# Kernel tuning notes

Hardware: AMD Instinct MI355X
Metric: run time of the kernel (lower is better)

## Reference

```python
import jax, jax.numpy as jnp
import numpy as np

B, C, H, W = 8, 96, 512, 96  # W == w_size (required by the view semantics)
EPS = 1e-5


def setup_inputs() -> dict:
    key = jax.random.key(0)
    ks = jax.random.split(key, 3)
    x = jax.random.normal(ks[0], (B, C, H, W), dtype=jnp.float32)
    bn_gamma = jnp.ones((C,), jnp.float32)
    bn_beta = jnp.zeros((C,), jnp.float32)
    bn_mean = jnp.zeros((C,), jnp.float32)   # BatchNorm running mean (eval mode)
    bn_var = jnp.ones((C,), jnp.float32)     # BatchNorm running var  (eval mode)
    qkv_w = jax.random.normal(ks[1], (3 * C, C), jnp.float32) * (1.0 / np.sqrt(C))
    qkv_b = jnp.zeros((3 * C,), jnp.float32)
    return {"x": x, "bn_gamma": bn_gamma, "bn_beta": bn_beta,
            "bn_mean": bn_mean, "bn_var": bn_var,
            "qkv_w": qkv_w, "qkv_b": qkv_b}


def reference(x, bn_gamma, bn_beta, bn_mean, bn_var, qkv_w, qkv_b):
    # BatchNorm2d (eval-mode affine normalize), fused scale/shift per channel
    inv = (bn_gamma / jnp.sqrt(bn_var + EPS))[:, None, None]
    xn = (x - bn_mean[:, None, None]) * inv + bn_beta[:, None, None]
    # 1x1 conv QKV projection: [b,c,h,w] -> [b,3c,h,w]
    qkv = jnp.einsum('bchw,oc->bohw', xn, qkv_w) + qkv_b[None, :, None, None]
    q, k, v = jnp.split(qkv, 3, axis=1)  # each [b,c,h,w]
    # per-row attention over the width axis (w == w_size)
    qp = jnp.transpose(q, (0, 2, 3, 1))  # [b,h,w,c]
    kp = jnp.transpose(k, (0, 2, 3, 1))  # [b,h,w,c]
    vp = jnp.transpose(v, (0, 2, 3, 1))  # [b,h,w,c]
    score = jnp.einsum('bhqc,bhkc->bhqk', qp, kp)  # [b,h,w,w]
    attn = jax.nn.softmax(score, axis=-1)
    xt = jnp.einsum('bhqk,bhkc->bhqc', attn, vp)   # [b,h,w,c]
    out = jnp.transpose(xt, (0, 3, 1, 2)) + x       # residual add, [b,c,h,w]
    return out
```

## Files before the change

kernel.cpp:

```cpp
#include <hip/hip_runtime.h>

#define C_ 96
#define H_ 512
#define W_ 96
#define HW_ 49152
#define CHW_ 4718592
#define PIT 104
#define REG 9984

typedef _Float16 f16x8 __attribute__((ext_vector_type(8)));
typedef _Float16 f16x4 __attribute__((ext_vector_type(4)));
typedef _Float16 f16x2 __attribute__((ext_vector_type(2)));
typedef float    f32x4 __attribute__((ext_vector_type(4)));
typedef int      i32x4 __attribute__((ext_vector_type(4)));

#define MFMA16 __builtin_amdgcn_mfma_f32_16x16x32_f16

#define BAR() do { __builtin_amdgcn_sched_barrier(0); \
                   asm volatile("s_waitcnt lgkmcnt(0)" ::: "memory"); \
                   __builtin_amdgcn_s_barrier(); \
                   __builtin_amdgcn_sched_barrier(0); } while (0)

__global__ void prep_kernel(const float* __restrict__ wq,
                            const float* __restrict__ gamma,
                            const float* __restrict__ beta,
                            const float* __restrict__ mean,
                            const float* __restrict__ var,
                            const float* __restrict__ qkvb,
                            _Float16* __restrict__ whf,
                            float* __restrict__ bprime)
{
    int i = blockIdx.x * 256 + threadIdx.x;
    if (i < 3 * C_ * C_) {
        int c = i % C_;
        float iv = gamma[c] * rsqrtf(var[c] + 1e-5f);
        whf[i] = (_Float16)(wq[i] * iv);
    }
    if (i < 3 * C_) {
        float acc = qkvb[i];
        for (int c = 0; c < C_; ++c) {
            float iv = gamma[c] * rsqrtf(var[c] + 1e-5f);
            acc += wq[i * C_ + c] * (beta[c] - mean[c] * iv);
        }
        bprime[i] = acc;
    }
}

__global__ void prep2_kernel(const float* __restrict__ wq,
                             const float* __restrict__ gamma,
                             const float* __restrict__ var,
                             const float* __restrict__ bprime,
                             _Float16* __restrict__ atm,
                             float* __restrict__ g0)
{
    int i = blockIdx.x * 256 + threadIdx.x;
    if (i >= 9216) return;
    int c = i / 96, cp = i % 96;
    float ivc  = gamma[c]  * rsqrtf(var[c]  + 1e-5f);
    float ivcp = gamma[cp] * rsqrtf(var[cp] + 1e-5f);
    float acc = 0.f;
    #pragma unroll 4
    for (int o = 0; o < 96; ++o)
        acc += wq[o * 96 + cp] * wq[(96 + o) * 96 + c];
    atm[c * 96 + cp] = (_Float16)(acc * ivc * ivcp);
    if (cp == 0) {
        float a2 = 0.f;
        #pragma unroll 4
        for (int o = 0; o < 96; ++o)
            a2 += bprime[o] * wq[(96 + o) * 96 + c];
        g0[c] = a2 * ivc;
    }
}

__device__ __forceinline__ void xchg(const f32x4 v[6], float scale,
                                     int q4, int n16, f16x8 fr[3])
{
    int pq[6][2];
    #pragma unroll
    for (int nt = 0; nt < 6; ++nt) {
        #pragma unroll
        for (int jj = 0; jj < 2; ++jj) {
            f16x2 h;
            h[0] = (_Float16)(v[nt][2 * jj] * scale);
            h[1] = (_Float16)(v[nt][2 * jj + 1] * scale);
            pq[nt][jj] = __builtin_bit_cast(int, h);
        }
    }
    const int srcA = ((q4 & 1) << 5) | n16;
    const int srcB = srcA + 16;
    #pragma unroll
    for (int kk = 0; kk < 3; ++kk) {
        const int a0 = __shfl(pq[2 * kk][0], srcA), a1 = __shfl(pq[2 * kk][1], srcA);
        const int a2 = __shfl(pq[2 * kk][0], srcB), a3 = __shfl(pq[2 * kk][1], srcB);
        const int b0 = __shfl(pq[2 * kk + 1][0], srcA), b1 = __shfl(pq[2 * kk + 1][1], srcA);
        const int b2 = __shfl(pq[2 * kk + 1][0], srcB), b3 = __shfl(pq[2 * kk + 1][1], srcB);
        i32x4 u;
        u[0] = (q4 < 2) ? a0 : b0;
        u[1] = (q4 < 2) ? a1 : b1;
        u[2] = (q4 < 2) ? a2 : b2;
        u[3] = (q4 < 2) ? a3 : b3;
        fr[kk] = __builtin_bit_cast(f16x8, u);
    }
}

__global__ __launch_bounds__(384, 5) void attn_kernel(
    const float* __restrict__ x,
    const _Float16* __restrict__ whf,
    const _Float16* __restrict__ atm,
    const float* __restrict__ g0,
    const float* __restrict__ bprime,
    float* __restrict__ out)
{
    __shared__ __align__(16) _Float16 smem[2 * REG];
    _Float16* XN  = smem;
    _Float16* XNT = smem + REG;

    const int tid  = threadIdx.x;
    const int ws   = tid >> 6;
    const int lane = tid & 63;
    const int q4   = lane >> 4;
    const int n16  = lane & 15;
    const int w0   = 16 * ws + 4 * q4;
    const int qrow = 16 * ws + n16;

    const int bh = blockIdx.x;
    const size_t base = (size_t)(bh >> 9) * CHW_ + (size_t)(bh & 511) * W_;

    {
        f32x4 xr[6];
        #pragma unroll
        for (int t = 0; t < 6; ++t)
            xr[t] = *(const f32x4*)(x + base + (size_t)(16 * t + n16) * HW_ + w0);
        #pragma unroll
        for (int t = 0; t < 6; ++t) {
            const int c = 16 * t + n16;
            f16x4 pk;
            #pragma unroll
            for (int r = 0; r < 4; ++r) pk[r] = (_Float16)xr[t][r];
            *(f16x4*)(XNT + c * PIT + w0) = pk;
            #pragma unroll
            for (int r = 0; r < 4; ++r)
                XN[(w0 + r) * PIT + c] = (_Float16)xr[t][r];
        }
    }
    BAR();

    f32x4 gac[6];
    #pragma unroll
    for (int nt = 0; nt < 6; ++nt)
        gac[nt] = *(const f32x4*)(g0 + 16 * nt + 4 * q4);
    #pragma unroll
    for (int kk = 0; kk < 3; ++kk) {
        const f16x8 bfr = *(const f16x8*)(XN + qrow * PIT + 32 * kk + 8 * q4);
        #pragma unroll
        for (int nt = 0; nt < 6; ++nt) {
            const f16x8 afr = *(const f16x8*)(atm + (16 * nt + n16) * 96 + 32 * kk + 8 * q4);
            gac[nt] = MFMA16(afr, bfr, gac[nt], 0, 0, 0);
        }
    }
    f16x8 gf[3];
    xchg(gac, 1.0f, q4, n16, gf);

    f32x4 sacc[6];
    #pragma unroll
    for (int nt = 0; nt < 6; ++nt) sacc[nt] = f32x4{0.f, 0.f, 0.f, 0.f};
    #pragma unroll
    for (int kk = 0; kk < 3; ++kk) {
        #pragma unroll
        for (int nt = 0; nt < 6; ++nt) {
            const f16x8 afr = *(const f16x8*)(XN + (16 * nt + n16) * PIT + 32 * kk + 8 * q4);
            sacc[nt] = MFMA16(afr, gf[kk], sacc[nt], 0, 0, 0);
        }
    }

    float mr0 = sacc[0][0], mr1 = sacc[0][1], mr2 = sacc[0][2], mr3 = sacc[0][3];
    #pragma unroll
    for (int nt = 1; nt < 6; ++nt) {
        mr0 = fmaxf(mr0, sacc[nt][0]); mr1 = fmaxf(mr1, sacc[nt][1]);
        mr2 = fmaxf(mr2, sacc[nt][2]); mr3 = fmaxf(mr3, sacc[nt][3]);
    }
    float m = fmaxf(fmaxf(mr0, mr1), fmaxf(mr2, mr3));
    m = fmaxf(m, __shfl_xor(m, 16));
    m = fmaxf(m, __shfl_xor(m, 32));
    float sr0 = 0.f, sr1 = 0.f, sr2 = 0.f, sr3 = 0.f;
    #pragma unroll
    for (int nt = 0; nt < 6; ++nt) {
        sacc[nt][0] = __expf(sacc[nt][0] - m); sr0 += sacc[nt][0];
        sacc[nt][1] = __expf(sacc[nt][1] - m); sr1 += sacc[nt][1];
        sacc[nt][2] = __expf(sacc[nt][2] - m); sr2 += sacc[nt][2];
        sacc[nt][3] = __expf(sacc[nt][3] - m); sr3 += sacc[nt][3];
    }
    float s = (sr0 + sr1) + (sr2 + sr3);
    s += __shfl_xor(s, 16);
    s += __shfl_xor(s, 32);
    const float pinv = 1.0f / s;

    f16x8 pa[3];
    xchg(sacc, pinv, q4, n16, pa);

    float xv[6][4];
    #pragma unroll
    for (int ot = 0; ot < 6; ++ot)
        #pragma unroll
        for (int r = 0; r < 4; ++r)
            xv[ot][r] = x[base + (size_t)(16 * ot + 4 * q4 + r) * HW_ + qrow];

    f32x4 zac[6];
    #pragma unroll
    for (int nt = 0; nt < 6; ++nt) zac[nt] = f32x4{0.f, 0.f, 0.f, 0.f};
    #pragma unroll
    for (int kk = 0; kk < 3; ++kk) {
        #pragma unroll
        for (int nt = 0; nt < 6; ++nt) {
            const f16x8 afr = *(const f16x8*)(XNT + (16 * nt + n16) * PIT + 32 * kk + 8 * q4);
            zac[nt] = MFMA16(afr, pa[kk], zac[nt], 0, 0, 0);
        }
    }
    f16x8 zf[3];
    xchg(zac, 1.0f, q4, n16, zf);

    f32x4 oacc[6];
    #pragma unroll
    for (int ot = 0; ot < 6; ++ot)
        oacc[ot] = *(const f32x4*)(bprime + 192 + 16 * ot + 4 * q4);
    #pragma unroll
    for (int kk = 0; kk < 3; ++kk) {
        #pragma unroll
        for (int ot = 0; ot < 6; ++ot) {
            const f16x8 afr = *(const f16x8*)(whf + (192 + 16 * ot + n16) * 96 + 32 * kk + 8 * q4);
            oacc[ot] = MFMA16(afr, zf[kk], oacc[ot], 0, 0, 0);
        }
    }

    #pragma unroll
    for (int ot = 0; ot < 6; ++ot)
        #pragma unroll
        for (int r = 0; r < 4; ++r)
            out[base + (size_t)(16 * ot + 4 * q4 + r) * HW_ + qrow] =
                oacc[ot][r] + xv[ot][r];
}

extern "C" void kernel_launch(void* const* d_in, const int* in_sizes, int n_in,
                              void* d_out, int out_size, void* d_ws, size_t ws_size,
                              hipStream_t stream)
{
    const float* x     = (const float*)d_in[0];
    const float* gamma = (const float*)d_in[1];
    const float* beta  = (const float*)d_in[2];
    const float* mean  = (const float*)d_in[3];
    const float* var   = (const float*)d_in[4];
    const float* qkvw  = (const float*)d_in[5];
    const float* qkvb  = (const float*)d_in[6];
    float* out = (float*)d_out;

    _Float16* whf    = (_Float16*)d_ws;
    float*    bprime = (float*)((char*)d_ws + 55296);
    _Float16* atm    = (_Float16*)((char*)d_ws + 56448);
    float*    g0v    = (float*)((char*)d_ws + 74880);

    prep_kernel<<<108, 256, 0, stream>>>(qkvw, gamma, beta, mean, var, qkvb, whf, bprime);
    prep2_kernel<<<36, 256, 0, stream>>>(qkvw, gamma, var, bprime, atm, g0v);
    attn_kernel<<<4096, 384, 0, stream>>>(x, whf, atm, g0v, bprime, out);
}
```

Baseline: 366.1 us.

## Switch to 16x16x16 MFMA so accumulator layouts feed next stage without shuffles

Replaces the 16x16x32 f16 MFMA chain with the 16x16x16 variant. Its output accumulator layout matches the B-operand layout of the next MFMA, so the cross-lane shuffle exchange (xchg) between the four GEMM stages becomes a plain f32-to-f16 conversion in registers. It also double-buffers the global weight-fragment loads for the first and last GEMMs. The cost is twice as many MFMA instructions and smaller 8-byte LDS and global fragment loads in exchange for removing the shuffles.

```diff
diff --git a/kernel.cpp b/kernel.cpp
--- a/kernel.cpp
+++ b/kernel.cpp
@@ -10,11 +10,9 @@
 
 typedef _Float16 f16x8 __attribute__((ext_vector_type(8)));
 typedef _Float16 f16x4 __attribute__((ext_vector_type(4)));
-typedef _Float16 f16x2 __attribute__((ext_vector_type(2)));
 typedef float    f32x4 __attribute__((ext_vector_type(4)));
-typedef int      i32x4 __attribute__((ext_vector_type(4)));
-
-#define MFMA16 __builtin_amdgcn_mfma_f32_16x16x32_f16
+
+#define MFMA16K __builtin_amdgcn_mfma_f32_16x16x16f16
 
 #define BAR() do { __builtin_amdgcn_sched_barrier(0); \
                    asm volatile("s_waitcnt lgkmcnt(0)" ::: "memory"); \
@@ -59,47 +57,16 @@
     float ivc  = gamma[c]  * rsqrtf(var[c]  + 1e-5f);
     float ivcp = gamma[cp] * rsqrtf(var[cp] + 1e-5f);
     float acc = 0.f;
-    #pragma unroll 4
+    #pragma unroll 8
     for (int o = 0; o < 96; ++o)
         acc += wq[o * 96 + cp] * wq[(96 + o) * 96 + c];
     atm[c * 96 + cp] = (_Float16)(acc * ivc * ivcp);
     if (cp == 0) {
         float a2 = 0.f;
-        #pragma unroll 4
+        #pragma unroll 8
         for (int o = 0; o < 96; ++o)
             a2 += bprime[o] * wq[(96 + o) * 96 + c];
         g0[c] = a2 * ivc;
-    }
-}
-
-__device__ __forceinline__ void xchg(const f32x4 v[6], float scale,
-                                     int q4, int n16, f16x8 fr[3])
-{
-    int pq[6][2];
-    #pragma unroll
-    for (int nt = 0; nt < 6; ++nt) {
-        #pragma unroll
-        for (int jj = 0; jj < 2; ++jj) {
-            f16x2 h;
-            h[0] = (_Float16)(v[nt][2 * jj] * scale);
-            h[1] = (_Float16)(v[nt][2 * jj + 1] * scale);
-            pq[nt][jj] = __builtin_bit_cast(int, h);
-        }
-    }
-    const int srcA = ((q4 & 1) << 5) | n16;
-    const int srcB = srcA + 16;
-    #pragma unroll
-    for (int kk = 0; kk < 3; ++kk) {
-        const int a0 = __shfl(pq[2 * kk][0], srcA), a1 = __shfl(pq[2 * kk][1], srcA);
-        const int a2 = __shfl(pq[2 * kk][0], srcB), a3 = __shfl(pq[2 * kk][1], srcB);
-        const int b0 = __shfl(pq[2 * kk + 1][0], srcA), b1 = __shfl(pq[2 * kk + 1][1], srcA);
-        const int b2 = __shfl(pq[2 * kk + 1][0], srcB), b3 = __shfl(pq[2 * kk + 1][1], srcB);
-        i32x4 u;
-        u[0] = (q4 < 2) ? a0 : b0;
-        u[1] = (q4 < 2) ? a1 : b1;
-        u[2] = (q4 < 2) ? a2 : b2;
-        u[3] = (q4 < 2) ? a3 : b3;
-        fr[kk] = __builtin_bit_cast(f16x8, u);
     }
 }
 
@@ -147,29 +114,43 @@
 
     f32x4 gac[6];
     #pragma unroll
-    for (int nt = 0; nt < 6; ++nt)
-        gac[nt] = *(const f32x4*)(g0 + 16 * nt + 4 * q4);
-    #pragma unroll
-    for (int kk = 0; kk < 3; ++kk) {
-        const f16x8 bfr = *(const f16x8*)(XN + qrow * PIT + 32 * kk + 8 * q4);
+    for (int ct = 0; ct < 6; ++ct)
+        gac[ct] = *(const f32x4*)(g0 + 16 * ct + 4 * q4);
+    {
+        f16x4 atf[2][6];
+        #pragma unroll
+        for (int ct = 0; ct < 6; ++ct)
+            atf[0][ct] = *(const f16x4*)(atm + (16 * ct + n16) * 96 + 4 * q4);
+        #pragma unroll
+        for (int kk = 0; kk < 6; ++kk) {
+            if (kk < 5) {
+                #pragma unroll
+                for (int ct = 0; ct < 6; ++ct)
+                    atf[(kk + 1) & 1][ct] =
+                        *(const f16x4*)(atm + (16 * ct + n16) * 96 + 16 * (kk + 1) + 4 * q4);
+            }
+            const f16x4 bq = *(const f16x4*)(XN + qrow * PIT + 16 * kk + 4 * q4);
+            #pragma unroll
+            for (int ct = 0; ct < 6; ++ct)
+                gac[ct] = MFMA16K(atf[kk & 1][ct], bq, gac[ct], 0, 0, 0);
+        }
+    }
+    f16x4 gf[6];
+    #pragma unroll
+    for (int ct = 0; ct < 6; ++ct) {
+        #pragma unroll
+        for (int r = 0; r < 4; ++r) gf[ct][r] = (_Float16)gac[ct][r];
+    }
+
+    f32x4 sacc[6];
+    #pragma unroll
+    for (int nt = 0; nt < 6; ++nt) sacc[nt] = f32x4{0.f, 0.f, 0.f, 0.f};
+    #pragma unroll
+    for (int kk = 0; kk < 6; ++kk) {
         #pragma unroll
         for (int nt = 0; nt < 6; ++nt) {
-            const f16x8 afr = *(const f16x8*)(atm + (16 * nt + n16) * 96 + 32 * kk + 8 * q4);
-            gac[nt] = MFMA16(afr, bfr, gac[nt], 0, 0, 0);
-        }
-    }
-    f16x8 gf[3];
-    xchg(gac, 1.0f, q4, n16, gf);
-
-    f32x4 sacc[6];
-    #pragma unroll
-    for (int nt = 0; nt < 6; ++nt) sacc[nt] = f32x4{0.f, 0.f, 0.f, 0.f};
-    #pragma unroll
-    for (int kk = 0; kk < 3; ++kk) {
-        #pragma unroll
-        for (int nt = 0; nt < 6; ++nt) {
-            const f16x8 afr = *(const f16x8*)(XN + (16 * nt + n16) * PIT + 32 * kk + 8 * q4);
-            sacc[nt] = MFMA16(afr, gf[kk], sacc[nt], 0, 0, 0);
+            const f16x4 a = *(const f16x4*)(XN + (16 * nt + n16) * PIT + 16 * kk + 4 * q4);
+            sacc[nt] = MFMA16K(a, gf[kk], sacc[nt], 0, 0, 0);
         }
     }
 
@@ -194,9 +175,30 @@
     s += __shfl_xor(s, 16);
     s += __shfl_xor(s, 32);
     const float pinv = 1.0f / s;
-
-    f16x8 pa[3];
-    xchg(sacc, pinv, q4, n16, pa);
+    f16x4 pb[6];
+    #pragma unroll
+    for (int kk = 0; kk < 6; ++kk) {
+        #pragma unroll
+        for (int r = 0; r < 4; ++r) pb[kk][r] = (_Float16)(sacc[kk][r] * pinv);
+    }
+
+    f32x4 zac[6];
+    #pragma unroll
+    for (int nt = 0; nt < 6; ++nt) zac[nt] = f32x4{0.f, 0.f, 0.f, 0.f};
+    #pragma unroll
+    for (int kk = 0; kk < 6; ++kk) {
+        #pragma unroll
+        for (int nt = 0; nt < 6; ++nt) {
+            const f16x4 a = *(const f16x4*)(XNT + (16 * nt + n16) * PIT + 16 * kk + 4 * q4);
+            zac[nt] = MFMA16K(a, pb[kk], zac[nt], 0, 0, 0);
+        }
+    }
+    f16x4 zf[6];
+    #pragma unroll
+    for (int ct = 0; ct < 6; ++ct) {
+        #pragma unroll
+        for (int r = 0; r < 4; ++r) zf[ct][r] = (_Float16)zac[ct][r];
+    }
 
     float xv[6][4];
     #pragma unroll
@@ -205,30 +207,26 @@
         for (int r = 0; r < 4; ++r)
             xv[ot][r] = x[base + (size_t)(16 * ot + 4 * q4 + r) * HW_ + qrow];
 
-    f32x4 zac[6];
-    #pragma unroll
-    for (int nt = 0; nt < 6; ++nt) zac[nt] = f32x4{0.f, 0.f, 0.f, 0.f};
-    #pragma unroll
-    for (int kk = 0; kk < 3; ++kk) {
-        #pragma unroll
-        for (int nt = 0; nt < 6; ++nt) {
-            const f16x8 afr = *(const f16x8*)(XNT + (16 * nt + n16) * PIT + 32 * kk + 8 * q4);
-            zac[nt] = MFMA16(afr, pa[kk], zac[nt], 0, 0, 0);
-        }
-    }
-    f16x8 zf[3];
-    xchg(zac, 1.0f, q4, n16, zf);
-
     f32x4 oacc[6];
     #pragma unroll
     for (int ot = 0; ot < 6; ++ot)
         oacc[ot] = *(const f32x4*)(bprime + 192 + 16 * ot + 4 * q4);
-    #pragma unroll
-    for (int kk = 0; kk < 3; ++kk) {
-        #pragma unroll
-        for (int ot = 0; ot < 6; ++ot) {
-            const f16x8 afr = *(const f16x8*)(whf + (192 + 16 * ot + n16) * 96 + 32 * kk + 8 * q4);
-            oacc[ot] = MFMA16(afr, zf[kk], oacc[ot], 0, 0, 0);
+    {
+        f16x4 wvf[2][6];
+        #pragma unroll
+        for (int ot = 0; ot < 6; ++ot)
+            wvf[0][ot] = *(const f16x4*)(whf + (192 + 16 * ot + n16) * 96 + 4 * q4);
+        #pragma unroll
+        for (int kk = 0; kk < 6; ++kk) {
+            if (kk < 5) {
+                #pragma unroll
+                for (int ot = 0; ot < 6; ++ot)
+                    wvf[(kk + 1) & 1][ot] =
+                        *(const f16x4*)(whf + (192 + 16 * ot + n16) * 96 + 16 * (kk + 1) + 4 * q4);
+            }
+            #pragma unroll
+            for (int ot = 0; ot < 6; ++ot)
+                oacc[ot] = MFMA16K(wvf[kk & 1][ot], zf[kk], oacc[ot], 0, 0, 0);
         }
     }
 
```

After: 407.5 us. +11.3%, slower.

## Process eight rows per block with double-buffered LDS and register-resident weights

Applied to the files above, without the earlier changes.

Each workgroup now handles eight consecutive h-rows instead of one. The next row's x is prefetched into registers during the current row's compute and staged into a second LDS buffer. The atm fragments are hoisted into registers once per block, and the residual is read from the fp16 LDS copy instead of reloading x from global memory. The aim is to amortise setup and hide global-load latency, at the cost of far fewer blocks (lower occupancy), higher register pressure, and reduced residual precision.

```diff
diff --git a/kernel.cpp b/kernel.cpp
--- a/kernel.cpp
+++ b/kernel.cpp
@@ -7,6 +7,7 @@
 #define CHW_ 4718592
 #define PIT 104
 #define REG 9984
+#define TILES 8
 
 typedef _Float16 f16x8 __attribute__((ext_vector_type(8)));
 typedef _Float16 f16x4 __attribute__((ext_vector_type(4)));
@@ -59,13 +60,13 @@
     float ivc  = gamma[c]  * rsqrtf(var[c]  + 1e-5f);
     float ivcp = gamma[cp] * rsqrtf(var[cp] + 1e-5f);
     float acc = 0.f;
-    #pragma unroll 4
+    #pragma unroll 8
     for (int o = 0; o < 96; ++o)
         acc += wq[o * 96 + cp] * wq[(96 + o) * 96 + c];
     atm[c * 96 + cp] = (_Float16)(acc * ivc * ivcp);
     if (cp == 0) {
         float a2 = 0.f;
-        #pragma unroll 4
+        #pragma unroll 8
         for (int o = 0; o < 96; ++o)
             a2 += bprime[o] * wq[(96 + o) * 96 + c];
         g0[c] = a2 * ivc;
@@ -103,7 +104,7 @@
     }
 }
 
-__global__ __launch_bounds__(384, 5) void attn_kernel(
+__global__ __launch_bounds__(384, 3) void attn_kernel(
     const float* __restrict__ x,
     const _Float16* __restrict__ whf,
     const _Float16* __restrict__ atm,
@@ -111,9 +112,7 @@
     const float* __restrict__ bprime,
     float* __restrict__ out)
 {
-    __shared__ __align__(16) _Float16 smem[2 * REG];
-    _Float16* XN  = smem;
-    _Float16* XNT = smem + REG;
+    __shared__ __align__(16) _Float16 smem[4 * REG];
 
     const int tid  = threadIdx.x;
     const int ws   = tid >> 6;
@@ -123,121 +122,155 @@
     const int w0   = 16 * ws + 4 * q4;
     const int qrow = 16 * ws + n16;
 
-    const int bh = blockIdx.x;
-    const size_t base = (size_t)(bh >> 9) * CHW_ + (size_t)(bh & 511) * W_;
+    const int wg = blockIdx.x;
+    size_t base = (size_t)(wg >> 6) * CHW_ + (size_t)((wg & 63) * TILES) * W_;
+
+    f16x8 atf[3][6];
+    #pragma unroll
+    for (int kk = 0; kk < 3; ++kk)
+        #pragma unroll
+        for (int nt = 0; nt < 6; ++nt)
+            atf[kk][nt] = *(const f16x8*)(atm + (16 * nt + n16) * 96 + 32 * kk + 8 * q4);
 
     {
         f32x4 xr[6];
         #pragma unroll
-        for (int t = 0; t < 6; ++t)
-            xr[t] = *(const f32x4*)(x + base + (size_t)(16 * t + n16) * HW_ + w0);
-        #pragma unroll
-        for (int t = 0; t < 6; ++t) {
-            const int c = 16 * t + n16;
+        for (int t6 = 0; t6 < 6; ++t6)
+            xr[t6] = *(const f32x4*)(x + base + (size_t)(16 * t6 + n16) * HW_ + w0);
+        #pragma unroll
+        for (int t6 = 0; t6 < 6; ++t6) {
+            const int c = 16 * t6 + n16;
             f16x4 pk;
             #pragma unroll
-            for (int r = 0; r < 4; ++r) pk[r] = (_Float16)xr[t][r];
-            *(f16x4*)(XNT + c * PIT + w0) = pk;
+            for (int r = 0; r < 4; ++r) pk[r] = (_Float16)xr[t6][r];
+            *(f16x4*)(smem + REG + c * PIT + w0) = pk;
             #pragma unroll
             for (int r = 0; r < 4; ++r)
-                XN[(w0 + r) * PIT + c] = (_Float16)xr[t][r];
+                smem[(w0 + r) * PIT + c] = (_Float16)xr[t6][r];
         }
     }
     BAR();
 
-    f32x4 gac[6];
-    #pragma unroll
-    for (int nt = 0; nt < 6; ++nt)
-        gac[nt] = *(const f32x4*)(g0 + 16 * nt + 4 * q4);
-    #pragma unroll
-    for (int kk = 0; kk < 3; ++kk) {
-        const f16x8 bfr = *(const f16x8*)(XN + qrow * PIT + 32 * kk + 8 * q4);
+    #pragma unroll 2
+    for (int t = 0; t < TILES; ++t) {
+        _Float16* XNc  = smem + ((t & 1) ? 2 * REG : 0);
+        _Float16* XNTc = XNc + REG;
+        _Float16* XNn  = smem + ((t & 1) ? 0 : 2 * REG);
+        _Float16* XNTn = XNn + REG;
+
+        f32x4 gac[6];
+        #pragma unroll
+        for (int nt = 0; nt < 6; ++nt)
+            gac[nt] = *(const f32x4*)(g0 + 16 * nt + 4 * q4);
+        #pragma unroll
+        for (int kk = 0; kk < 3; ++kk) {
+            const f16x8 bq = *(const f16x8*)(XNc + qrow * PIT + 32 * kk + 8 * q4);
+            #pragma unroll
+            for (int nt = 0; nt < 6; ++nt)
+                gac[nt] = MFMA16(atf[kk][nt], bq, gac[nt], 0, 0, 0);
+        }
+        f16x8 gf[3];
+        xchg(gac, 1.0f, q4, n16, gf);
+
+        f32x4 sacc[6];
+        #pragma unroll
+        for (int nt = 0; nt < 6; ++nt) sacc[nt] = f32x4{0.f, 0.f, 0.f, 0.f};
+        #pragma unroll
+        for (int kk = 0; kk < 3; ++kk) {
+            #pragma unroll
+            for (int nt = 0; nt < 6; ++nt) {
+                const f16x8 a = *(const f16x8*)(XNc + (16 * nt + n16) * PIT + 32 * kk + 8 * q4);
+                sacc[nt] = MFMA16(a, gf[kk], sacc[nt], 0, 0, 0);
+            }
+        }
+
+        float mr0 = sacc[0][0], mr1 = sacc[0][1], mr2 = sacc[0][2], mr3 = sacc[0][3];
+        #pragma unroll
+        for (int nt = 1; nt < 6; ++nt) {
+            mr0 = fmaxf(mr0, sacc[nt][0]); mr1 = fmaxf(mr1, sacc[nt][1]);
+            mr2 = fmaxf(mr2, sacc[nt][2]); mr3 = fmaxf(mr3, sacc[nt][3]);
+        }
+        float m = fmaxf(fmaxf(mr0, mr1), fmaxf(mr2, mr3));
+        m = fmaxf(m, __shfl_xor(m, 16));
+        m = fmaxf(m, __shfl_xor(m, 32));
+        float sr0 = 0.f, sr1 = 0.f, sr2 = 0.f, sr3 = 0.f;
         #pragma unroll
         for (int nt = 0; nt < 6; ++nt) {
-            const f16x8 afr = *(const f16x8*)(atm + (16 * nt + n16) * 96 + 32 * kk + 8 * q4);
-            gac[nt] = MFMA16(afr, bfr, gac[nt], 0, 0, 0);
-        }
-    }
-    f16x8 gf[3];
-    xchg(gac, 1.0f, q4, n16, gf);
-
-    f32x4 sacc[6];
-    #pragma unroll
-    for (int nt = 0; nt < 6; ++nt) sacc[nt] = f32x4{0.f, 0.f, 0.f, 0.f};
-    #pragma unroll
-    for (int kk = 0; kk < 3; ++kk) {
-        #pragma unroll
-        for (int nt = 0; nt < 6; ++nt) {
-            const f16x8 afr = *(const f16x8*)(XN + (16 * nt + n16) * PIT + 32 * kk + 8 * q4);
-            sacc[nt] = MFMA16(afr, gf[kk], sacc[nt], 0, 0, 0);
-        }
-    }
-
-    float mr0 = sacc[0][0], mr1 = sacc[0][1], mr2 = sacc[0][2], mr3 = sacc[0][3];
-    #pragma unroll
-    for (int nt = 1; nt < 6; ++nt) {
-        mr0 = fmaxf(mr0, sacc[nt][0]); mr1 = fmaxf(mr1, sacc[nt][1]);
-        mr2 = fmaxf(mr2, sacc[nt][2]); mr3 = fmaxf(mr3, sacc[nt][3]);
-    }
-    float m = fmaxf(fmaxf(mr0, mr1), fmaxf(mr2, mr3));
-    m = fmaxf(m, __shfl_xor(m, 16));
-    m = fmaxf(m, __shfl_xor(m, 32));
-    float sr0 = 0.f, sr1 = 0.f, sr2 = 0.f, sr3 = 0.f;
-    #pragma unroll
-    for (int nt = 0; nt < 6; ++nt) {
-        sacc[nt][0] = __expf(sacc[nt][0] - m); sr0 += sacc[nt][0];
-        sacc[nt][1] = __expf(sacc[nt][1] - m); sr1 += sacc[nt][1];
-        sacc[nt][2] = __expf(sacc[nt][2] - m); sr2 += sacc[nt][2];
-        sacc[nt][3] = __expf(sacc[nt][3] - m); sr3 += sacc[nt][3];
-    }
-    float s = (sr0 + sr1) + (sr2 + sr3);
-    s += __shfl_xor(s, 16);
-    s += __shfl_xor(s, 32);
-    const float pinv = 1.0f / s;
-
-    f16x8 pa[3];
-    xchg(sacc, pinv, q4, n16, pa);
-
-    float xv[6][4];
-    #pragma unroll
-    for (int ot = 0; ot < 6; ++ot)
-        #pragma unroll
-        for (int r = 0; r < 4; ++r)
-            xv[ot][r] = x[base + (size_t)(16 * ot + 4 * q4 + r) * HW_ + qrow];
-
-    f32x4 zac[6];
-    #pragma unroll
-    for (int nt = 0; nt < 6; ++nt) zac[nt] = f32x4{0.f, 0.f, 0.f, 0.f};
-    #pragma unroll
-    for (int kk = 0; kk < 3; ++kk) {
-        #pragma unroll
-        for (int nt = 0; nt < 6; ++nt) {
-            const f16x8 afr = *(const f16x8*)(XNT + (16 * nt + n16) * PIT + 32 * kk + 8 * q4);
-            zac[nt] = MFMA16(afr, pa[kk], zac[nt], 0, 0, 0);
-        }
-    }
-    f16x8 zf[3];
-    xchg(zac, 1.0f, q4, n16, zf);
-
-    f32x4 oacc[6];
-    #pragma unroll
-    for (int ot = 0; ot < 6; ++ot)
-        oacc[ot] = *(const f32x4*)(bprime + 192 + 16 * ot + 4 * q4);
-    #pragma unroll
-    for (int kk = 0; kk < 3; ++kk) {
+            sacc[nt][0] = __expf(sacc[nt][0] - m); sr0 += sacc[nt][0];
+            sacc[nt][1] = __expf(sacc[nt][1] - m); sr1 += sacc[nt][1];
+            sacc[nt][2] = __expf(sacc[nt][2] - m); sr2 += sacc[nt][2];
+            sacc[nt][3] = __expf(sacc[nt][3] - m); sr3 += sacc[nt][3];
+        }
+        float s = (sr0 + sr1) + (sr2 + sr3);
+        s += __shfl_xor(s, 16);
+        s += __shfl_xor(s, 32);
+        const float pinv = 1.0f / s;
+        f16x8 pa[3];
+        xchg(sacc, pinv, q4, n16, pa);
+
+        f32x4 xrn[6];
+        if (t < TILES - 1) {
+            #pragma unroll
+            for (int t6 = 0; t6 < 6; ++t6)
+                xrn[t6] = *(const f32x4*)(x + base + W_
+                              + (size_t)(16 * t6 + n16) * HW_ + w0);
+        }
+
+        f32x4 zac[6];
+        #pragma unroll
+        for (int nt = 0; nt < 6; ++nt) zac[nt] = f32x4{0.f, 0.f, 0.f, 0.f};
+        #pragma unroll
+        for (int kk = 0; kk < 3; ++kk) {
+            #pragma unroll
+            for (int nt = 0; nt < 6; ++nt) {
+                const f16x8 a = *(const f16x8*)(XNTc + (16 * nt + n16) * PIT + 32 * kk + 8 * q4);
+                zac[nt] = MFMA16(a, pa[kk], zac[nt], 0, 0, 0);
+            }
+        }
+        f16x8 zf[3];
+        xchg(zac, 1.0f, q4, n16, zf);
+
+        f32x4 oacc[6];
+        #pragma unroll
+        for (int ot = 0; ot < 6; ++ot)
+            oacc[ot] = *(const f32x4*)(bprime + 192 + 16 * ot + 4 * q4);
+        #pragma unroll
+        for (int kk = 0; kk < 3; ++kk) {
+            f16x8 wv[6];
+            #pragma unroll
+            for (int ot = 0; ot < 6; ++ot)
+                wv[ot] = *(const f16x8*)(whf + (192 + 16 * ot + n16) * 96 + 32 * kk + 8 * q4);
+            #pragma unroll
+            for (int ot = 0; ot < 6; ++ot)
+                oacc[ot] = MFMA16(wv[ot], zf[kk], oacc[ot], 0, 0, 0);
+        }
+
         #pragma unroll
         for (int ot = 0; ot < 6; ++ot) {
-            const f16x8 afr = *(const f16x8*)(whf + (192 + 16 * ot + n16) * 96 + 32 * kk + 8 * q4);
-            oacc[ot] = MFMA16(afr, zf[kk], oacc[ot], 0, 0, 0);
-        }
-    }
-
-    #pragma unroll
-    for (int ot = 0; ot < 6; ++ot)
-        #pragma unroll
-        for (int r = 0; r < 4; ++r)
-            out[base + (size_t)(16 * ot + 4 * q4 + r) * HW_ + qrow] =
-                oacc[ot][r] + xv[ot][r];
+            #pragma unroll
+            for (int r = 0; r < 4; ++r) {
+                const float xv = (float)XNTc[(16 * ot + 4 * q4 + r) * PIT + qrow];
+                out[base + (size_t)(16 * ot + 4 * q4 + r) * HW_ + qrow] =
+                    oacc[ot][r] + xv;
+            }
+        }
+
+        if (t < TILES - 1) {
+            #pragma unroll
+            for (int t6 = 0; t6 < 6; ++t6) {
+                const int c = 16 * t6 + n16;
+                f16x4 pk;
+                #pragma unroll
+                for (int r = 0; r < 4; ++r) pk[r] = (_Float16)xrn[t6][r];
+                *(f16x4*)(XNTn + c * PIT + w0) = pk;
+                #pragma unroll
+                for (int r = 0; r < 4; ++r)
+                    XNn[(w0 + r) * PIT + c] = (_Float16)xrn[t6][r];
+            }
+            base += W_;
+            BAR();
+        }
+    }
 }
 
 extern "C" void kernel_launch(void* const* d_in, const int* in_sizes, int n_in,
@@ -260,5 +293,5 @@
 
     prep_kernel<<<108, 256, 0, stream>>>(qkvw, gamma, beta, mean, var, qkvb, whf, bprime);
     prep2_kernel<<<36, 256, 0, stream>>>(qkvw, gamma, var, bprime, atm, g0v);
-    attn_kernel<<<4096, 384, 0, stream>>>(x, whf, atm, g0v, bprime, out);
-}
+    attn_kernel<<<512, 384, 0, stream>>>(x, whf, atm, g0v, bprime, out);
+}
```

After: 608.1 us. 66.1% more time.

## Parallelize weight prep kernels and read residual from shared-memory x tile

Applied to the files above, without the earlier changes.

The prep stage is split into three kernels. Per-channel BN scale/shift are computed once, the folded bias becomes a wave-level shuffle reduction, and the attention-matrix precompute gives each block one channel, with the key column staged in shared memory. This removes serial loops over 96 channels per thread. The main kernel now takes the residual from the fp16 x tile already in LDS instead of reloading x from global memory, which saves a second global read but rounds the residual to fp16. An extra kernel launch is added.

```diff
diff --git a/kernel.cpp b/kernel.cpp
--- a/kernel.cpp
+++ b/kernel.cpp
@@ -26,9 +26,9 @@
                             const float* __restrict__ beta,
                             const float* __restrict__ mean,
                             const float* __restrict__ var,
-                            const float* __restrict__ qkvb,
                             _Float16* __restrict__ whf,
-                            float* __restrict__ bprime)
+                            float* __restrict__ inv,
+                            float* __restrict__ shift)
 {
     int i = blockIdx.x * 256 + threadIdx.x;
     if (i < 3 * C_ * C_) {
@@ -36,39 +36,54 @@
         float iv = gamma[c] * rsqrtf(var[c] + 1e-5f);
         whf[i] = (_Float16)(wq[i] * iv);
     }
-    if (i < 3 * C_) {
-        float acc = qkvb[i];
-        for (int c = 0; c < C_; ++c) {
-            float iv = gamma[c] * rsqrtf(var[c] + 1e-5f);
-            acc += wq[i * C_ + c] * (beta[c] - mean[c] * iv);
-        }
-        bprime[i] = acc;
-    }
+    if (i < C_) {
+        float iv = gamma[i] * rsqrtf(var[i] + 1e-5f);
+        inv[i]   = iv;
+        shift[i] = beta[i] - mean[i] * iv;
+    }
+}
+
+__global__ void prep_bias(const float* __restrict__ wq,
+                          const float* __restrict__ qkvb,
+                          const float* __restrict__ shift,
+                          float* __restrict__ bprime)
+{
+    const int o = (blockIdx.x * 256 + threadIdx.x) >> 6;
+    const int l = threadIdx.x & 63;
+    if (o >= 3 * C_) return;
+    float p = wq[o * C_ + l] * shift[l];
+    if (l < 32) p += wq[o * C_ + 64 + l] * shift[64 + l];
+    #pragma unroll
+    for (int d = 32; d >= 1; d >>= 1) p += __shfl_xor(p, d);
+    if (l == 0) bprime[o] = p + qkvb[o];
 }
 
 __global__ void prep2_kernel(const float* __restrict__ wq,
-                             const float* __restrict__ gamma,
-                             const float* __restrict__ var,
+                             const float* __restrict__ inv,
                              const float* __restrict__ bprime,
                              _Float16* __restrict__ atm,
                              float* __restrict__ g0)
 {
-    int i = blockIdx.x * 256 + threadIdx.x;
-    if (i >= 9216) return;
-    int c = i / 96, cp = i % 96;
-    float ivc  = gamma[c]  * rsqrtf(var[c]  + 1e-5f);
-    float ivcp = gamma[cp] * rsqrtf(var[cp] + 1e-5f);
-    float acc = 0.f;
-    #pragma unroll 4
-    for (int o = 0; o < 96; ++o)
-        acc += wq[o * 96 + cp] * wq[(96 + o) * 96 + c];
-    atm[c * 96 + cp] = (_Float16)(acc * ivc * ivcp);
-    if (cp == 0) {
-        float a2 = 0.f;
-        #pragma unroll 4
-        for (int o = 0; o < 96; ++o)
-            a2 += bprime[o] * wq[(96 + o) * 96 + c];
-        g0[c] = a2 * ivc;
+    const int c = blockIdx.x;
+    const int t = threadIdx.x;
+    __shared__ float ldsk[C_];
+    if (t < C_) ldsk[t] = wq[(C_ + t) * C_ + c];
+    __syncthreads();
+    const float ivc = inv[c];
+    if (t < C_) {
+        float acc = 0.f;
+        #pragma unroll 8
+        for (int o = 0; o < C_; ++o)
+            acc += wq[o * C_ + t] * ldsk[o];
+        atm[c * C_ + t] = (_Float16)(acc * ivc * inv[t]);
+    }
+    if (t >= 64) {
+        const int l = t - 64;
+        float p = bprime[l] * ldsk[l];
+        if (l < 32) p += bprime[64 + l] * ldsk[64 + l];
+        #pragma unroll
+        for (int d = 32; d >= 1; d >>= 1) p += __shfl_xor(p, d);
+        if (l == 0) g0[c] = p * ivc;
     }
 }
 
@@ -198,13 +213,6 @@
     f16x8 pa[3];
     xchg(sacc, pinv, q4, n16, pa);
 
-    float xv[6][4];
-    #pragma unroll
-    for (int ot = 0; ot < 6; ++ot)
-        #pragma unroll
-        for (int r = 0; r < 4; ++r)
-            xv[ot][r] = x[base + (size_t)(16 * ot + 4 * q4 + r) * HW_ + qrow];
-
     f32x4 zac[6];
     #pragma unroll
     for (int nt = 0; nt < 6; ++nt) zac[nt] = f32x4{0.f, 0.f, 0.f, 0.f};
@@ -233,11 +241,14 @@
     }
 
     #pragma unroll
-    for (int ot = 0; ot < 6; ++ot)
-        #pragma unroll
-        for (int r = 0; r < 4; ++r)
+    for (int ot = 0; ot < 6; ++ot) {
+        #pragma unroll
+        for (int r = 0; r < 4; ++r) {
+            const float xv = (float)XNT[(16 * ot + 4 * q4 + r) * PIT + qrow];
             out[base + (size_t)(16 * ot + 4 * q4 + r) * HW_ + qrow] =
-                oacc[ot][r] + xv[ot][r];
+                oacc[ot][r] + xv;
+        }
+    }
 }
 
 extern "C" void kernel_launch(void* const* d_in, const int* in_sizes, int n_in,
@@ -257,8 +268,11 @@
     float*    bprime = (float*)((char*)d_ws + 55296);
     _Float16* atm    = (_Float16*)((char*)d_ws + 56448);
     float*    g0v    = (float*)((char*)d_ws + 74880);
-
-    prep_kernel<<<108, 256, 0, stream>>>(qkvw, gamma, beta, mean, var, qkvb, whf, bprime);
-    prep2_kernel<<<36, 256, 0, stream>>>(qkvw, gamma, var, bprime, atm, g0v);
+    float*    inv    = (float*)((char*)d_ws + 75264);
+    float*    shf    = (float*)((char*)d_ws + 75648);
+
+    prep_kernel<<<108, 256, 0, stream>>>(qkvw, gamma, beta, mean, var, whf, inv, shf);
+    prep_bias <<<72, 256, 0, stream>>>(qkvw, qkvb, shf, bprime);
+    prep2_kernel<<<96, 128, 0, stream>>>(qkvw, inv, bprime, atm, g0v);
     attn_kernel<<<4096, 384, 0, stream>>>(x, whf, atm, g0v, bprime, out);
 }
```

New measurement: 325.2 us. -11.2%, faster.
